# Kernel optimization log

Hardware: AMD Instinct MI355X
Metric: run time of the kernel (lower is better)

The kernel has to match this reference:

```python
import jax, jax.numpy as jnp
import numpy as np


def setup_inputs() -> dict:
    key = jax.random.key(0)
    n, d = 256, 64
    ks = jax.random.split(key, 8)
    x = jax.random.normal(ks[0], (n, d), jnp.float32)
    v = jax.random.normal(ks[1], (n, d), jnp.float32)
    # torch nn.Linear convention: weight shape (out_features, in_features)
    W1 = jax.random.normal(ks[2], (d, d), jnp.float32) * (1.0 / np.sqrt(d))
    b1 = jax.random.normal(ks[3], (d,), jnp.float32) * 0.1
    # W2 scaled small + b2 ~ scaled identity so g = M + M^T is well-conditioned (invertible)
    W2 = jax.random.normal(ks[4], (d * d, d), jnp.float32) * 0.02
    b2 = (3.0 * jnp.eye(d, dtype=jnp.float32)).reshape(d * d) \
         + jax.random.normal(ks[5], (d * d,), jnp.float32) * 0.01
    W3 = jax.random.normal(ks[6], (d, 2 * d), jnp.float32) * (1.0 / np.sqrt(2 * d))
    return {"t": 0, "x": x, "v": v, "W1": W1, "b1": b1, "W2": W2, "b2": b2, "W3": W3}


def reference(t, x, v, W1, b1, W2, b2, W3):
    # Connection_gnew.forward. t is unused (ODE-time placeholder), matching the original.
    n, d = x.shape
    # g network: linear1 -> tanh -> linear2 -> symmetrize
    h = jnp.tanh(x @ W1.T + b1)                      # (n, d)
    M = (h @ W2.T + b2).reshape(n, d, d)             # (n, d, d)
    g = M + jnp.transpose(M, (0, 2, 1))              # symmetric metric (n, d, d)
    g_inv = jnp.linalg.inv(g)
    # Analytic batch jacobian of g_flat wrt x (replaces autograd.functional.jacobian):
    # d M_flat[a]/d x[l] = sum_m W2[a,m] * (1 - h[m]^2) * W1[m,l]; then symmetrize (i<->j).
    s = 1.0 - h * h                                   # tanh' (n, d)
    J = jnp.einsum('am,nm,ml->nal', W2, s, W1).reshape(n, d, d, d)
    J = J + jnp.transpose(J, (0, 2, 1, 3))            # J[n,i,j,l] = d g_{ij} / d x_l
    # einsum('nkl,nijl,njil,nlij->nkij', g_inv, J, J, -J):
    # elementwise triple product over matching indices, then contract l with g_inv.
    T = J * jnp.transpose(J, (0, 2, 1, 3)) * (-jnp.transpose(J, (0, 2, 3, 1)))  # T[n,i,j,l]
    connection = 0.5 * jnp.einsum('nkl,nijl->nkij', g_inv, T)
    # dv[n,k] = -sum_{ij} v_i v_j connection[n,k,i,j]
    dv = -jnp.einsum('ni,nj,nkij->nk', v, v, connection)
    out = jnp.concatenate([v, dv], axis=-1) @ W3.T    # linear3, no bias
    return out
```

## Files before the change

kernel.cpp:

```cpp
#include <hip/hip_runtime.h>
#include <math.h>
#include <stdint.h>


typedef short short8 __attribute__((ext_vector_type(8)));
typedef float f32x4 __attribute__((ext_vector_type(4)));

__device__ __forceinline__ unsigned short f2bf(float f) {
  unsigned int u = __builtin_bit_cast(unsigned int, f);
  u += 0x7fffu + ((u >> 16) & 1u);
  return (unsigned short)(u >> 16);
}

__device__ __forceinline__ short8 as_short8(uint4 u) {
  union { uint4 a; short8 b; } cv; cv.a = u; return cv.b;
}

__global__ __launch_bounds__(256) void prep_w2s_kernel(const float* __restrict__ W2,
                                                       unsigned short* __restrict__ W2sB) {
  int g = blockIdx.x * 256 + threadIdx.x;
  int i = g >> 9, j = (g >> 3) & 63, m8 = (g & 7) << 3;
  const float* pa = &W2[((((i << 6) + j) << 6) + m8)];
  const float* pb = &W2[((((j << 6) + i) << 6) + m8)];
  float4 a0 = *(const float4*)pa, a1 = *(const float4*)(pa + 4);
  float4 b0 = *(const float4*)pb, b1 = *(const float4*)(pb + 4);
  short8 r;
  r[0] = (short)f2bf(a0.x + b0.x); r[1] = (short)f2bf(a0.y + b0.y);
  r[2] = (short)f2bf(a0.z + b0.z); r[3] = (short)f2bf(a0.w + b0.w);
  r[4] = (short)f2bf(a1.x + b1.x); r[5] = (short)f2bf(a1.y + b1.y);
  r[6] = (short)f2bf(a1.z + b1.z); r[7] = (short)f2bf(a1.w + b1.w);
  *(short8*)&W2sB[(size_t)g << 3] = r;
}

__global__ __launch_bounds__(512) void conn_kernel(
    const float* __restrict__ x, const float* __restrict__ v,
    const float* __restrict__ W1, const float* __restrict__ b1,
    const float* __restrict__ b2, const float* __restrict__ W3,
    const unsigned short* __restrict__ W2sB, float* __restrict__ out) {
  __shared__ __align__(16) unsigned short sKT[80 * 80];
  __shared__ __align__(16) float sg[64 * 68];
  __shared__ float spq[8][64];
  __shared__ __align__(16) float sh[64], sv[64], sx[64], sq[64];
  __shared__ __align__(16) float sz2[2][64];

  const int n = blockIdx.x, t = threadIdx.x;
  const int wv = t >> 6, lane = t & 63, ln15 = lane & 15, quad = lane >> 4;
  const int o8 = t >> 3, s8 = t & 7;

  if (t < 64) sx[t] = x[(n << 6) + t];
  else if (t < 128) sv[t - 64] = v[(n << 6) + (t - 64)];
  for (int e = t; e < 1280; e += 512) sKT[5120 + e] = 0;
  __syncthreads();

  {
    const float* w1r = &W1[(o8 << 6) + (s8 << 3)];
    float4 wa = *(const float4*)w1r, wb = *(const float4*)(w1r + 4);
    float4 xa = *(const float4*)&sx[s8 << 3], xb = *(const float4*)&sx[(s8 << 3) + 4];
    float acc = wa.x * xa.x + wa.y * xa.y + wa.z * xa.z + wa.w * xa.w
              + wb.x * xb.x + wb.y * xb.y + wb.z * xb.z + wb.w * xb.w;
    acc += __shfl_xor(acc, 1);
    acc += __shfl_xor(acc, 2);
    acc += __shfl_xor(acc, 4);
    if (s8 == 0) sh[o8] = tanhf(acc + b1[o8]);
  }
  __syncthreads();

  for (int e = t; e < 4096; e += 512) {
    int m = e & 63, l = e >> 6;
    float hm = sh[m];
    sKT[l * 80 + m] = f2bf((1.f - hm * hm) * W1[(m << 6) + l]);
  }
  if (t < 64) sKT[64 * 80 + t] = f2bf(sh[t]);
  __syncthreads();

  short8 bf[4][2];
  #pragma unroll
  for (int tc = 0; tc < 4; ++tc)
    #pragma unroll
    for (int ks = 0; ks < 2; ++ks)
      bf[tc][ks] = *(const short8*)&sKT[(tc * 16 + ln15) * 80 + ks * 32 + quad * 8];

  float qacc[4] = {0.f, 0.f, 0.f, 0.f};

  const int foff = (ln15 << 6) + quad * 8;
  const int extoff = (64 + ln15) * 80 + quad * 8;
  const unsigned short* sbase = W2sB + ((size_t)(8 * wv) << 12);

  #pragma unroll 1
  for (int ii = 0; ii < 8; ++ii) {
    const unsigned short* sp = sbase + ((size_t)ii << 12);
    uint4 af[4][2];
    #pragma unroll
    for (int tc = 0; tc < 4; ++tc) {
      af[tc][0] = *(const uint4*)(sp + (tc << 10) + foff);
      af[tc][1] = *(const uint4*)(sp + (tc << 10) + foff + 32);
    }
    const int i = 8 * wv + ii;
    const float vi = sv[i];

    #pragma unroll
    for (int tr = 0; tr < 4; ++tr) {
      short8 a0 = as_short8(af[tr][0]), a1 = as_short8(af[tr][1]);
      f32x4 svj = *(const f32x4*)&sv[tr * 16 + quad * 4];
      {
        short8 e0 = *(const short8*)&sKT[extoff];
        short8 e1 = *(const short8*)&sKT[extoff + 32];
        f32x4 z4 = {0.f, 0.f, 0.f, 0.f};
        f32x4 u  = __builtin_amdgcn_mfma_f32_16x16x32_bf16(a0, e0, z4, 0, 0, 0);
        f32x4 ce = __builtin_amdgcn_mfma_f32_16x16x32_bf16(a1, e1, u, 0, 0, 0);
        if (ln15 == 0)
          *(f32x4*)&sg[i * 68 + tr * 16 + quad * 4] = ce;
      }
      #pragma unroll
      for (int tc = 0; tc < 4; ++tc) {
        f32x4 z4 = {0.f, 0.f, 0.f, 0.f};
        f32x4 u  = __builtin_amdgcn_mfma_f32_16x16x32_bf16(a0, bf[tc][0], z4, 0, 0, 0);
        f32x4 c1 = __builtin_amdgcn_mfma_f32_16x16x32_bf16(a1, bf[tc][1], u, 0, 0, 0);
        f32x4 w  = __builtin_amdgcn_mfma_f32_16x16x32_bf16(bf[tr][0], as_short8(af[tc][0]), z4, 0, 0, 0);
        f32x4 c2 = __builtin_amdgcn_mfma_f32_16x16x32_bf16(bf[tr][1], as_short8(af[tc][1]), w, 0, 0, 0);
        float s = 0.f;
        #pragma unroll
        for (int r = 0; r < 4; ++r) {
          float a = c1[r];
          s = fmaf(a * a * c2[r], svj[r], s);
        }
        qacc[tc] = fmaf(s, vi, qacc[tc]);
      }
    }
  }

  #pragma unroll
  for (int tc = 0; tc < 4; ++tc) {
    float s = qacc[tc];
    s += __shfl_xor(s, 16, 64);
    s += __shfl_xor(s, 32, 64);
    if (quad == 0) spq[wv][tc * 16 + ln15] = s;
  }
  __syncthreads();

  for (int e = t; e < 4096; e += 512) {
    int r = e >> 6, c = e & 63;
    sg[r * 68 + c] += b2[(r << 6) + c] + b2[(c << 6) + r];
  }
  __syncthreads();

  if (t < 64) {
    float s = spq[0][t] + spq[1][t] + spq[2][t] + spq[3][t]
            + spq[4][t] + spq[5][t] + spq[6][t] + spq[7][t];
    sq[t] = s;
    sz2[0][t] = s / sg[t * 68 + t];
  }
  __syncthreads();

  {
    const int row = o8;
    const float* grow = &sg[row * 68];
    const float dinv = 1.f / grow[row];
    const float qr = sq[row];
    int pb = 0;
    for (int it = 0; it < 20; ++it) {
      float p = 0.f;
      #pragma unroll
      for (int cc = 0; cc < 8; ++cc) {
        int c = (cc << 3) + s8;
        p += grow[c] * sz2[pb][c];
      }
      p += __shfl_xor(p, 1);
      p += __shfl_xor(p, 2);
      p += __shfl_xor(p, 4);
      if (s8 == 0) sz2[pb ^ 1][row] = sz2[pb][row] + (qr - p) * dinv;
      __syncthreads();
      pb ^= 1;
    }
  }

  {
    const float* w3r = &W3[o8 << 7];
    float4 wva = *(const float4*)&w3r[s8 << 3];
    float4 wvb = *(const float4*)&w3r[(s8 << 3) + 4];
    float4 wda = *(const float4*)&w3r[64 + (s8 << 3)];
    float4 wdb = *(const float4*)&w3r[64 + (s8 << 3) + 4];
    float4 va = *(const float4*)&sv[s8 << 3], vb = *(const float4*)&sv[(s8 << 3) + 4];
    float4 za = *(const float4*)&sz2[0][s8 << 3], zb = *(const float4*)&sz2[0][(s8 << 3) + 4];
    float acc = wva.x * va.x + wva.y * va.y + wva.z * va.z + wva.w * va.w
              + wvb.x * vb.x + wvb.y * vb.y + wvb.z * vb.z + wvb.w * vb.w
              + 0.5f * (wda.x * za.x + wda.y * za.y + wda.z * za.z + wda.w * za.w
                      + wdb.x * zb.x + wdb.y * zb.y + wdb.z * zb.z + wdb.w * zb.w);
    acc += __shfl_xor(acc, 1);
    acc += __shfl_xor(acc, 2);
    acc += __shfl_xor(acc, 4);
    if (s8 == 0) out[(n << 6) + o8] = acc;
  }
}

extern "C" void kernel_launch(void* const* d_in, const int* in_sizes, int n_in,
                              void* d_out, int out_size, void* d_ws, size_t ws_size,
                              hipStream_t stream) {
  (void)in_sizes; (void)n_in; (void)out_size; (void)ws_size;
  const float* x  = (const float*)d_in[1];
  const float* v  = (const float*)d_in[2];
  const float* W1 = (const float*)d_in[3];
  const float* b1 = (const float*)d_in[4];
  const float* W2 = (const float*)d_in[5];
  const float* b2 = (const float*)d_in[6];
  const float* W3 = (const float*)d_in[7];
  unsigned short* W2sB = (unsigned short*)d_ws;

  hipLaunchKernelGGL(prep_w2s_kernel, dim3(128), dim3(256), 0, stream, W2, W2sB);
  hipLaunchKernelGGL(conn_kernel, dim3(256), dim3(512), 0, stream,
                     x, v, W1, b1, b2, W3, W2sB, (float*)d_out);
}
```

Baseline: 101.3 us.

## Double-buffer W2 slabs into LDS via async global_load_lds with XOR swizzle

```diff
diff --git a/kernel.cpp b/kernel.cpp
--- a/kernel.cpp
+++ b/kernel.cpp
@@ -14,6 +14,19 @@
 
 __device__ __forceinline__ short8 as_short8(uint4 u) {
   union { uint4 a; short8 b; } cv; cv.a = u; return cv.b;
+}
+
+__device__ __forceinline__ void stage_slab(const unsigned short* gslab,
+                                           unsigned short* lbase, int lane) {
+  const int srcoff = ((lane >> 3) << 6) + (((lane & 7) ^ (lane >> 3)) << 3);
+  const unsigned short* gsrc = gslab + srcoff;
+  #pragma unroll
+  for (int k = 0; k < 8; ++k) {
+    __builtin_amdgcn_global_load_lds(
+        (const __attribute__((address_space(1))) unsigned int*)(gsrc + (k << 9)),
+        (__attribute__((address_space(3))) unsigned int*)(lbase + (k << 9)),
+        16, 0, 0);
+  }
 }
 
 __global__ __launch_bounds__(256) void prep_w2s_kernel(const float* __restrict__ W2,
@@ -37,11 +50,14 @@
     const float* __restrict__ W1, const float* __restrict__ b1,
     const float* __restrict__ b2, const float* __restrict__ W3,
     const unsigned short* __restrict__ W2sB, float* __restrict__ out) {
+  __shared__ __align__(16) unsigned short sAF[8][2][4096];
   __shared__ __align__(16) unsigned short sKT[80 * 80];
   __shared__ __align__(16) float sg[64 * 68];
-  __shared__ float spq[8][64];
-  __shared__ __align__(16) float sh[64], sv[64], sx[64], sq[64];
-  __shared__ __align__(16) float sz2[2][64];
+  __shared__ __align__(16) float sh[64], sv[64], sx[64];
+
+  float* const spq = (float*)sKT;
+  float* const sq  = (float*)sKT + 512;
+  float* const szz = (float*)sKT + 576;
 
   const int n = blockIdx.x, t = threadIdx.x;
   const int wv = t >> 6, lane = t & 63, ln15 = lane & 15, quad = lane >> 4;
@@ -82,18 +98,26 @@
 
   float qacc[4] = {0.f, 0.f, 0.f, 0.f};
 
-  const int foff = (ln15 << 6) + quad * 8;
+  const int f0 = (ln15 << 6) + (((quad ^ ln15) & 7) << 3);
   const int extoff = (64 + ln15) * 80 + quad * 8;
-  const unsigned short* sbase = W2sB + ((size_t)(8 * wv) << 12);
+  unsigned short* const myAF = &sAF[wv][0][0];
+  const unsigned short* const gbase = W2sB + ((size_t)(8 * wv) << 12);
+
+  stage_slab(gbase, myAF, lane);
 
   #pragma unroll 1
   for (int ii = 0; ii < 8; ++ii) {
-    const unsigned short* sp = sbase + ((size_t)ii << 12);
+    asm volatile("s_waitcnt vmcnt(0)" ::: "memory");
+    __builtin_amdgcn_sched_barrier(0);
+    if (ii < 7)
+      stage_slab(gbase + ((size_t)(ii + 1) << 12), myAF + (((ii & 1) ^ 1) << 12), lane);
+
+    const unsigned short* buf = myAF + ((ii & 1) << 12);
     uint4 af[4][2];
     #pragma unroll
     for (int tc = 0; tc < 4; ++tc) {
-      af[tc][0] = *(const uint4*)(sp + (tc << 10) + foff);
-      af[tc][1] = *(const uint4*)(sp + (tc << 10) + foff + 32);
+      af[tc][0] = *(const uint4*)&buf[(tc << 10) + f0];
+      af[tc][1] = *(const uint4*)&buf[(tc << 10) + (f0 ^ 32)];
     }
     const int i = 8 * wv + ii;
     const float vi = sv[i];
@@ -134,7 +158,7 @@
     float s = qacc[tc];
     s += __shfl_xor(s, 16, 64);
     s += __shfl_xor(s, 32, 64);
-    if (quad == 0) spq[wv][tc * 16 + ln15] = s;
+    if (quad == 0) spq[(wv << 6) + tc * 16 + ln15] = s;
   }
   __syncthreads();
 
@@ -145,10 +169,10 @@
   __syncthreads();
 
   if (t < 64) {
-    float s = spq[0][t] + spq[1][t] + spq[2][t] + spq[3][t]
-            + spq[4][t] + spq[5][t] + spq[6][t] + spq[7][t];
+    float s = spq[t] + spq[64 + t] + spq[128 + t] + spq[192 + t]
+            + spq[256 + t] + spq[320 + t] + spq[384 + t] + spq[448 + t];
     sq[t] = s;
-    sz2[0][t] = s / sg[t * 68 + t];
+    szz[t] = s / sg[t * 68 + t];
   }
   __syncthreads();
 
@@ -163,12 +187,12 @@
       #pragma unroll
       for (int cc = 0; cc < 8; ++cc) {
         int c = (cc << 3) + s8;
-        p += grow[c] * sz2[pb][c];
+        p += grow[c] * szz[(pb << 6) + c];
       }
       p += __shfl_xor(p, 1);
       p += __shfl_xor(p, 2);
       p += __shfl_xor(p, 4);
-      if (s8 == 0) sz2[pb ^ 1][row] = sz2[pb][row] + (qr - p) * dinv;
+      if (s8 == 0) szz[((pb ^ 1) << 6) + row] = szz[(pb << 6) + row] + (qr - p) * dinv;
       __syncthreads();
       pb ^= 1;
     }
@@ -181,7 +205,7 @@
     float4 wda = *(const float4*)&w3r[64 + (s8 << 3)];
     float4 wdb = *(const float4*)&w3r[64 + (s8 << 3) + 4];
     float4 va = *(const float4*)&sv[s8 << 3], vb = *(const float4*)&sv[(s8 << 3) + 4];
-    float4 za = *(const float4*)&sz2[0][s8 << 3], zb = *(const float4*)&sz2[0][(s8 << 3) + 4];
+    float4 za = *(const float4*)&szz[s8 << 3], zb = *(const float4*)&szz[(s8 << 3) + 4];
     float acc = wva.x * va.x + wva.y * va.y + wva.z * va.z + wva.w * va.w
               + wvb.x * vb.x + wvb.y * vb.y + wvb.z * vb.z + wvb.w * vb.w
               + 0.5f * (wda.x * za.x + wda.y * za.y + wda.z * za.z + wda.w * za.w
```

After: 101.2 us. No clear change (-0.1%).
